# Kernel optimization log

Hardware: AMD Instinct MI355X
Metric: run time of the kernel (lower is better)

The kernel has to match this reference:

```python
import jax, jax.numpy as jnp
import numpy as np

H, W, C, HEADS = 28, 28, 512, 16
N = H * W
FF = 4 * C
DH = C // HEADS
NUM_REL = (2 * H - 1) * W + (2 * W - 1) + 1  # max relative index + 1 (source table is under-sized; see notes)


def _relative_indices():
    ys, xs = np.meshgrid(np.arange(H), np.arange(W), indexing='ij')
    py, px = ys.reshape(-1), xs.reshape(-1)
    # rel[q, k] = (y_k - y_q + H) * W + (x_k - x_q + W), matching the source loop
    rel = (py[None, :] - py[:, None] + H) * W + (px[None, :] - px[:, None] + W)
    return jnp.asarray(rel, dtype=jnp.int32)  # (N, N)


def setup_inputs() -> dict:
    key = jax.random.key(0)
    ks = jax.random.split(key, 9)
    g = lambda k, shape, s: (jax.random.normal(k, shape, jnp.float32) * s)
    return {
        'x': g(ks[0], (16, C, H, W), 1.0),
        'ln_w': jnp.ones((C,), jnp.float32),
        'ln_b': jnp.zeros((C,), jnp.float32),
        'Wq': g(ks[1], (C, C), 0.02), 'bq': jnp.zeros((C,), jnp.float32),
        'Wk': g(ks[2], (C, C), 0.02), 'bk': jnp.zeros((C,), jnp.float32),
        'Wv': g(ks[3], (C, C), 0.02), 'bv': jnp.zeros((C,), jnp.float32),
        'Wo': g(ks[4], (C, C), 0.02), 'bo': jnp.zeros((C,), jnp.float32),
        'rel_bias': g(ks[5], (HEADS, NUM_REL), 0.02),
        'W1': g(ks[6], (C, FF), 0.02), 'b1': jnp.zeros((FF,), jnp.float32),
        'W2': g(ks[7], (FF, C), 0.02), 'b2': jnp.zeros((C,), jnp.float32),
        'rel_idx': _relative_indices(),
    }


def reference(x, ln_w, ln_b, Wq, bq, Wk, bk, Wv, bv, Wo, bo, rel_bias, W1, b1, W2, b2, rel_idx):
    b = x.shape[0]
    xc = jnp.transpose(x, (0, 2, 3, 1)).reshape(b, N, C)  # b n c
    # LayerNorm over channels (per spatial position)
    mu = xc.mean(-1, keepdims=True)
    var = jnp.mean(jnp.square(xc - mu), -1, keepdims=True)
    xn = (xc - mu) * jax.lax.rsqrt(var + 1e-5) * ln_w + ln_b

    split = lambda t: t.reshape(b, N, HEADS, DH).transpose(0, 2, 1, 3)  # b h n d
    q = split(xn @ Wq + bq)
    k = split(xn @ Wk + bk)
    v = split(xn @ Wv + bv)

    bias = rel_bias[:, rel_idx]  # gather -> (heads, n, n)
    scores = jnp.einsum('bhnd,bhmd->bhnm', q, k) + bias[None]  # no 1/sqrt(d), faithful to source
    attn = jax.nn.softmax(scores, axis=-1)
    out = jnp.einsum('bhnm,bhmd->bhnd', attn, v)
    out = out.transpose(0, 2, 1, 3).reshape(b, N, C) @ Wo + bo

    x1 = xc + out  # skip (Identity) + attention branch
    ff = jax.nn.gelu(x1 @ W1 + b1, approximate=False) @ W2 + b2
    x2 = x1 + ff
    return x2.reshape(b, H, W, C).transpose(0, 3, 1, 2)  # back to b c h w
```

## Files before the change

### kernel.cpp

```cpp
#include <hip/hip_runtime.h>
#include <hip/hip_bf16.h>
#include <math.h>
#include <stdint.h>


typedef __bf16 bf16;
typedef __attribute__((ext_vector_type(8))) __bf16 bf16x8;
typedef __attribute__((ext_vector_type(4))) __bf16 bf16x4;
typedef __attribute__((ext_vector_type(4))) float f32x4;

#define NN 784
#define CC 512
#define NHEADS 16
#define DHEAD 32
#define FFD 2048
#define NBATCH 16
#define NREL 1596
#define MFULL (NBATCH * NN)
#define PACKSZ ((size_t)6422528)

__global__ __launch_bounds__(256) void detect_dtype(const unsigned int* xw, int* flag)
{
  __shared__ int cnt[256];
  int plausible = 0;
  for (int i = threadIdx.x; i < 1024; i += 256) {
    unsigned w = xw[i];
    unsigned lo = w & 0xFFFFu;
    unsigned e = (lo >> 7) & 0xFFu;
    if (lo == 0u || (e >= 90u && e <= 140u)) plausible++;
  }
  cnt[threadIdx.x] = plausible;
  __syncthreads();
  if (threadIdx.x == 0) {
    int tot = 0;
    for (int i = 0; i < 256; i++) tot += cnt[i];
    flag[0] = (tot >= 768) ? 1 : 0;
  }
}


__global__ __launch_bounds__(256) void transpose_split_all(
    const float* __restrict__ Wq, const float* __restrict__ Wk,
    const float* __restrict__ Wv, const float* __restrict__ Wo,
    const float* __restrict__ W1, const float* __restrict__ W2,
    bf16* __restrict__ WqkvT_h, bf16* __restrict__ WqkvT_l,
    bf16* __restrict__ WoT_h,   bf16* __restrict__ WoT_l,
    bf16* __restrict__ W1T_h,   bf16* __restrict__ W1T_l,
    bf16* __restrict__ W2T_h,   bf16* __restrict__ W2T_l,
    const int* __restrict__ flag)
{
  if (flag[0] != 0) return;
  int id = blockIdx.x;
  const float* W; bf16 *th, *tl; int K, Nout, roff, nx;
  if (id < 256)       { W = Wq; th = WqkvT_h; tl = WqkvT_l; K = 512;  Nout = 512;  roff = 0;    nx = 16; }
  else if (id < 512)  { W = Wk; th = WqkvT_h; tl = WqkvT_l; K = 512;  Nout = 512;  roff = 512;  nx = 16; id -= 256; }
  else if (id < 768)  { W = Wv; th = WqkvT_h; tl = WqkvT_l; K = 512;  Nout = 512;  roff = 1024; nx = 16; id -= 512; }
  else if (id < 1024) { W = Wo; th = WoT_h;   tl = WoT_l;   K = 512;  Nout = 512;  roff = 0;    nx = 16; id -= 768; }
  else if (id < 2048) { W = W1; th = W1T_h;   tl = W1T_l;   K = 512;  Nout = 2048; roff = 0;    nx = 64; id -= 1024; }
  else                { W = W2; th = W2T_h;   tl = W2T_l;   K = 2048; Nout = 512;  roff = 0;    nx = 16; id -= 2048; }
  const int n0 = (id % nx) * 32, k0 = (id / nx) * 32;

  __shared__ float tile[32][33];
  int tx = threadIdx.x & 31, ty = threadIdx.x >> 5;
  #pragma unroll
  for (int r = 0; r < 32; r += 8)
    tile[ty + r][tx] = W[(size_t)(k0 + ty + r) * Nout + n0 + tx];
  __syncthreads();
  #pragma unroll
  for (int r = 0; r < 32; r += 8) {
    float v = tile[tx][ty + r];
    bf16 h = (bf16)v;
    float lo = v - (float)h;
    size_t idx = (size_t)(roff + n0 + ty + r) * K + k0 + tx;
    th[idx] = h;
    tl[idx] = (bf16)lo;
  }
}

__global__ __launch_bounds__(256) void ln_single(
    const float* __restrict__ x, const float* __restrict__ lnw,
    const float* __restrict__ lnb, bf16* __restrict__ xh,
    const int* __restrict__ flag)
{
  if (flag[0] != 0) return;
  int bn = blockIdx.x;
  int b = bn / NN, n = bn - b * NN;
  const float* xb = x + (size_t)b * CC * NN + n;
  int t = threadIdx.x;
  float v0 = xb[(size_t)t * NN];
  float v1 = xb[(size_t)(t + 256) * NN];
  float s = v0 + v1, ss = v0 * v0 + v1 * v1;
  #pragma unroll
  for (int m = 32; m >= 1; m >>= 1) {
    s  += __shfl_xor(s,  m);
    ss += __shfl_xor(ss, m);
  }
  __shared__ float red[2][4];
  int w = t >> 6, l = t & 63;
  if (l == 0) { red[0][w] = s; red[1][w] = ss; }
  __syncthreads();
  float S  = red[0][0] + red[0][1] + red[0][2] + red[0][3];
  float SS = red[1][0] + red[1][1] + red[1][2] + red[1][3];
  float mu  = S * (1.f / 512.f);
  float var = SS * (1.f / 512.f) - mu * mu;
  float rstd = rsqrtf(var + 1e-5f);
  size_t o = (size_t)bn * CC;
  xh[o + t]       = (bf16)(((v0 - mu) * rstd) * lnw[t]       + lnb[t]);
  xh[o + t + 256] = (bf16)(((v1 - mu) * rstd) * lnw[t + 256] + lnb[t + 256]);
}

template <int NOUT, int KD, int ACT, int RESM, int OUTM>
__global__ __launch_bounds__(256) void gemm2(
    const bf16* __restrict__ A,
    const bf16* __restrict__ Bh, const bf16* __restrict__ Bl,
    const float* __restrict__ bias_q, const float* __restrict__ bias_k,
    const float* __restrict__ bias_v,
    float* __restrict__ outf, bf16* __restrict__ out_hi, bf16* __restrict__ out_lo,
    const float* __restrict__ extra_f, const bf16* __restrict__ ex_hi,
    const bf16* __restrict__ ex_lo,
    int M, const int* __restrict__ flag)
{
  if (flag[0] != 0) return;
  __shared__ bf16 sA [2][128 * 32];
  __shared__ bf16 sBh[2][128 * 32];
  __shared__ bf16 sBl[2][128 * 32];
  const int t = threadIdx.x;
  const int lane = t & 63;
  const int w = t >> 6;
  const int wr = w >> 1, wc = w & 1;
  const int lr = lane & 15, kg = lane >> 4;

  int wg = blockIdx.y * gridDim.x + blockIdx.x;
  const int nwg = gridDim.x * gridDim.y;
  if ((nwg & 7) == 0) {
    const int cpx = nwg >> 3;
    wg = (wg & 7) * cpx + (wg >> 3);
  }
  const int tile_n = (wg % gridDim.x) * 128;
  const int tile_m = (wg / gridDim.x) * 128;

  f32x4 acc[4][4];
  #pragma unroll
  for (int m = 0; m < 4; m++)
    #pragma unroll
    for (int n = 0; n < 4; n++) acc[m][n] = (f32x4)0.f;

  const int s0 = t, s1 = t + 256;
  int ar0 = tile_m + (s0 >> 2); if (ar0 >= M) ar0 = M - 1;
  int ar1 = tile_m + (s1 >> 2); if (ar1 >= M) ar1 = M - 1;
  const int br0 = tile_n + (s0 >> 2);
  const int br1 = tile_n + (s1 >> 2);
  const int ac0 = (s0 & 3) * 8, ac1 = (s1 & 3) * 8;
  const size_t a0 = (size_t)ar0 * KD + ac0;
  const size_t a1 = (size_t)ar1 * KD + ac1;
  const size_t b0 = (size_t)br0 * KD + ac0;
  const size_t b1 = (size_t)br1 * KD + ac1;

  #define STAGE(BUF, KO)                                                      \
    do {                                                                      \
      __builtin_amdgcn_global_load_lds(                                       \
          (const __attribute__((address_space(1))) void*)(A + a0 + (KO)),     \
          (__attribute__((address_space(3))) void*)(sA[BUF] + s0 * 8), 16, 0, 0); \
      __builtin_amdgcn_global_load_lds(                                       \
          (const __attribute__((address_space(1))) void*)(A + a1 + (KO)),     \
          (__attribute__((address_space(3))) void*)(sA[BUF] + s1 * 8), 16, 0, 0); \
      __builtin_amdgcn_global_load_lds(                                       \
          (const __attribute__((address_space(1))) void*)(Bh + b0 + (KO)),    \
          (__attribute__((address_space(3))) void*)(sBh[BUF] + s0 * 8), 16, 0, 0); \
      __builtin_amdgcn_global_load_lds(                                       \
          (const __attribute__((address_space(1))) void*)(Bh + b1 + (KO)),    \
          (__attribute__((address_space(3))) void*)(sBh[BUF] + s1 * 8), 16, 0, 0); \
      __builtin_amdgcn_global_load_lds(                                       \
          (const __attribute__((address_space(1))) void*)(Bl + b0 + (KO)),    \
          (__attribute__((address_space(3))) void*)(sBl[BUF] + s0 * 8), 16, 0, 0); \
      __builtin_amdgcn_global_load_lds(                                       \
          (const __attribute__((address_space(1))) void*)(Bl + b1 + (KO)),    \
          (__attribute__((address_space(3))) void*)(sBl[BUF] + s1 * 8), 16, 0, 0); \
    } while (0)

  STAGE(0, 0);
  asm volatile("s_waitcnt vmcnt(0)" ::: "memory");
  __builtin_amdgcn_sched_barrier(0);
  __builtin_amdgcn_s_barrier();
  __builtin_amdgcn_sched_barrier(0);

  int cur = 0;
  for (int k0 = 0; k0 < KD; k0 += 32) {
    if (k0 + 32 < KD) {
      if (cur) STAGE(0, k0 + 32); else STAGE(1, k0 + 32);
    }
    const bf16* pA  = sA [cur];
    const bf16* pBh = sBh[cur];
    const bf16* pBl = sBl[cur];
    bf16x8 af[4], bh[4], bl[4];
    #pragma unroll
    for (int m = 0; m < 4; m++) {
      const int off = (wr * 64 + m * 16 + lr) * 32 + kg * 8;
      af[m] = *(const bf16x8*)(pA + off);
    }
    #pragma unroll
    for (int n = 0; n < 4; n++) {
      const int off = (wc * 64 + n * 16 + lr) * 32 + kg * 8;
      bh[n] = *(const bf16x8*)(pBh + off);
      bl[n] = *(const bf16x8*)(pBl + off);
    }
    #pragma unroll
    for (int m = 0; m < 4; m++)
      #pragma unroll
      for (int n = 0; n < 4; n++) {
        acc[m][n] = __builtin_amdgcn_mfma_f32_16x16x32_bf16(af[m], bh[n], acc[m][n], 0, 0, 0);
        acc[m][n] = __builtin_amdgcn_mfma_f32_16x16x32_bf16(af[m], bl[n], acc[m][n], 0, 0, 0);
      }
    asm volatile("s_waitcnt vmcnt(0)" ::: "memory");
    __builtin_amdgcn_sched_barrier(0);
    __builtin_amdgcn_s_barrier();
    __builtin_amdgcn_sched_barrier(0);
    cur ^= 1;
  }
  #undef STAGE

  #pragma unroll
  for (int m = 0; m < 4; m++) {
    const int r0 = tile_m + wr * 64 + m * 16 + kg * 4;
    #pragma unroll
    for (int n = 0; n < 4; n++) {
      const int cg = tile_n + wc * 64 + n * 16 + lr;
      float bv;
      if (OUTM == 5) {
        const int reg2 = cg >> 9;
        const float* bp = reg2 == 0 ? bias_q : (reg2 == 1 ? bias_k : bias_v);
        bv = bp[cg & 511];
      } else {
        bv = bias_q[cg];
      }
      #pragma unroll
      for (int j = 0; j < 4; j++) {
        const int rg = r0 + j;
        if (rg >= M) continue;
        float vacc = acc[m][n][j] + bv;
        if (ACT == 1) vacc = 0.5f * vacc * (1.f + erff(vacc * 0.70710678118654752f));
        if (RESM == 1) {
          int bl_ = rg / NN, nn = rg - bl_ * NN;
          vacc += extra_f[((size_t)bl_ * CC + cg) * NN + nn];
        }
        if (RESM == 2) {
          size_t ei = (size_t)rg * CC + cg;
          vacc += (float)ex_hi[ei] + (float)ex_lo[ei];
        }
        if (OUTM == 3) {
          size_t oi = (size_t)rg * NOUT + cg;
          bf16 h = (bf16)vacc;
          out_hi[oi] = h;
          out_lo[oi] = (bf16)(vacc - (float)h);
        } else if (OUTM == 4) {
          int bl_ = rg / NN, nn = rg - bl_ * NN;
          outf[((size_t)bl_ * CC + cg) * NN + nn] = vacc;
        } else if (OUTM == 6) {
          out_hi[(size_t)rg * NOUT + cg] = (bf16)vacc;
        } else if (OUTM == 5) {
          const int reg2 = cg >> 9;
          const int c = cg & 511;
          const int hh = c >> 5, dd = c & 31;
          const int bl_ = rg / NN, nn = rg - bl_ * NN;
          const int bh_ = bl_ * NHEADS + hh;
          bf16 h = (bf16)vacc;
          if (reg2 == 0) {
            out_hi[((size_t)bh_ * NN + nn) * 32 + dd] = h;
          } else if (reg2 == 1) {
            out_hi[PACKSZ + ((size_t)bh_ * NN + nn) * 32 + dd] = h;
          } else {
            out_hi[2 * PACKSZ + ((size_t)bh_ * 32 + dd) * NN + nn] = h;
          }
        }
      }
    }
  }
}

__global__ __launch_bounds__(256) void attn_mfma(
    const bf16* __restrict__ pack, const float* __restrict__ relb,
    bf16* __restrict__ o_out, const int* __restrict__ flag)
{
  if (flag[0] != 0) return;
  const int h = blockIdx.y, b = blockIdx.z;
  __shared__ float biasLds[NREL];
  for (int i = threadIdx.x; i < NREL; i += 256) biasLds[i] = relb[(size_t)h * NREL + i];
  __syncthreads();
  const int w = threadIdx.x >> 6, lane = threadIdx.x & 63;
  const int qtile = blockIdx.x * 4 + w;
  if (qtile >= 49) return;
  const int kg = lane >> 4, lq = lane & 15;
  const int qg = qtile * 16 + lq;
  const int bh = b * NHEADS + h;
  const bf16* Q  = pack;
  const bf16* K  = pack + PACKSZ;
  const bf16* Vt = pack + 2 * PACKSZ;
  __shared__ bf16 Plds[4][16][72];

  const bf16x8 qf = *(const bf16x8*)(Q + ((size_t)bh * NN + qg) * 32 + kg * 8);

  float m = -1e30f, l = 0.f;
  f32x4 o0 = (f32x4)0.f, o1 = (f32x4)0.f;
  const float* bb = biasLds + 812 - qg;
  const size_t vrow0 = ((size_t)bh * 32 + lq) * NN;
  const size_t vrow1 = ((size_t)bh * 32 + 16 + lq) * NN;

  for (int c = 0; c < 12; c++) {
    const int c0 = c * 64;
    f32x4 st[4];
    #pragma unroll
    for (int t = 0; t < 4; t++) {
      const int kvr = c0 + t * 16 + lq;
      const bf16x8 kf = *(const bf16x8*)(K + ((size_t)bh * NN + kvr) * 32 + kg * 8);
      st[t] = __builtin_amdgcn_mfma_f32_16x16x32_bf16(kf, qf, (f32x4)0.f, 0, 0, 0);
    }
    float cm = -1e30f;
    #pragma unroll
    for (int t = 0; t < 4; t++)
      #pragma unroll
      for (int r = 0; r < 4; r++) {
        st[t][r] += bb[c0 + t * 16 + 4 * kg + r];
        cm = fmaxf(cm, st[t][r]);
      }
    cm = fmaxf(cm, __shfl_xor(cm, 16));
    cm = fmaxf(cm, __shfl_xor(cm, 32));
    const float mn = fmaxf(m, cm);
    const float al = __expf(m - mn);
    m = mn;
    float cl = 0.f;
    #pragma unroll
    for (int t = 0; t < 4; t++) {
      bf16x4 pk;
      #pragma unroll
      for (int r = 0; r < 4; r++) {
        float p = __expf(st[t][r] - m);
        bf16 pb = (bf16)p;
        pk[r] = pb;
        cl += (float)pb;
      }
      *(bf16x4*)(&Plds[w][lq][t * 16 + 4 * kg]) = pk;
    }
    cl += __shfl_xor(cl, 16);
    cl += __shfl_xor(cl, 32);
    l = l * al + cl;
    #pragma unroll
    for (int r = 0; r < 4; r++) {
      const float ar = __shfl(al, (lane & 48) | (kg * 4 + r));
      o0[r] *= ar; o1[r] *= ar;
    }
    #pragma unroll
    for (int s2 = 0; s2 < 2; s2++) {
      const bf16x8 pa = *(const bf16x8*)(&Plds[w][lq][s2 * 32 + kg * 8]);
      const bf16x8 v0 = *(const bf16x8*)(Vt + vrow0 + c0 + s2 * 32 + kg * 8);
      const bf16x8 v1 = *(const bf16x8*)(Vt + vrow1 + c0 + s2 * 32 + kg * 8);
      o0 = __builtin_amdgcn_mfma_f32_16x16x32_bf16(pa, v0, o0, 0, 0, 0);
      o1 = __builtin_amdgcn_mfma_f32_16x16x32_bf16(pa, v1, o1, 0, 0, 0);
    }
  }

  {
    const int c0 = 768;
    const int kvr = c0 + lq;
    const bf16x8 kf = *(const bf16x8*)(K + ((size_t)bh * NN + kvr) * 32 + kg * 8);
    f32x4 a = __builtin_amdgcn_mfma_f32_16x16x32_bf16(kf, qf, (f32x4)0.f, 0, 0, 0);
    float cm = -1e30f;
    #pragma unroll
    for (int r = 0; r < 4; r++) {
      a[r] += bb[c0 + 4 * kg + r];
      cm = fmaxf(cm, a[r]);
    }
    cm = fmaxf(cm, __shfl_xor(cm, 16));
    cm = fmaxf(cm, __shfl_xor(cm, 32));
    const float mn = fmaxf(m, cm);
    const float al = __expf(m - mn);
    m = mn;
    float cl = 0.f;
    bf16x4 pk, zk;
    #pragma unroll
    for (int r = 0; r < 4; r++) {
      float p = __expf(a[r] - m);
      bf16 pb = (bf16)p;
      pk[r] = pb;
      zk[r] = (bf16)0.f;
      cl += (float)pb;
    }
    *(bf16x4*)(&Plds[w][lq][4 * kg]) = pk;
    *(bf16x4*)(&Plds[w][lq][16 + 4 * kg]) = zk;
    cl += __shfl_xor(cl, 16);
    cl += __shfl_xor(cl, 32);
    l = l * al + cl;
    #pragma unroll
    for (int r = 0; r < 4; r++) {
      const float ar = __shfl(al, (lane & 48) | (kg * 4 + r));
      o0[r] *= ar; o1[r] *= ar;
    }
    bf16x8 vz;
    #pragma unroll
    for (int e = 0; e < 8; e++) vz[e] = (bf16)0.f;
    const int voff = c0 + (kg < 2 ? kg * 8 : 0);
    bf16x8 v0 = *(const bf16x8*)(Vt + vrow0 + voff);
    bf16x8 v1 = *(const bf16x8*)(Vt + vrow1 + voff);
    if (kg >= 2) { v0 = vz; v1 = vz; }
    const bf16x8 pa = *(const bf16x8*)(&Plds[w][lq][kg * 8]);
    o0 = __builtin_amdgcn_mfma_f32_16x16x32_bf16(pa, v0, o0, 0, 0, 0);
    o1 = __builtin_amdgcn_mfma_f32_16x16x32_bf16(pa, v1, o1, 0, 0, 0);
  }

  const float inv = 1.f / l;
  #pragma unroll
  for (int r = 0; r < 4; r++) {
    const float ir = __shfl(inv, (lane & 48) | (kg * 4 + r));
    const int rq = qtile * 16 + kg * 4 + r;
    const size_t oi = ((size_t)b * NN + rq) * CC + h * DHEAD;
    o_out[oi + lq]      = (bf16)(o0[r] * ir);
    o_out[oi + 16 + lq] = (bf16)(o1[r] * ir);
  }
}

static void run_fast_fp32(void* const* d_in, void* d_out, char* base,
                          const int* flag, hipStream_t stream)
{
  const float* x    = (const float*)d_in[0];
  const float* lnw  = (const float*)d_in[1];
  const float* lnb  = (const float*)d_in[2];
  const float* Wq   = (const float*)d_in[3];
  const float* bq   = (const float*)d_in[4];
  const float* Wk   = (const float*)d_in[5];
  const float* bk   = (const float*)d_in[6];
  const float* Wv   = (const float*)d_in[7];
  const float* bv   = (const float*)d_in[8];
  const float* Wo   = (const float*)d_in[9];
  const float* bo   = (const float*)d_in[10];
  const float* relb = (const float*)d_in[11];
  const float* W1   = (const float*)d_in[12];
  const float* b1   = (const float*)d_in[13];
  const float* W2   = (const float*)d_in[14];
  const float* b2   = (const float*)d_in[15];
  float* outp = (float*)d_out;

  bf16* WqkvT_h = (bf16*)(base);
  bf16* WqkvT_l = WqkvT_h + (size_t)1536 * 512;
  bf16* WoT_h   = WqkvT_l + (size_t)1536 * 512;
  bf16* WoT_l   = WoT_h   + (size_t)512 * 512;
  bf16* W1T_h   = WoT_l   + (size_t)512 * 512;
  bf16* W1T_l   = W1T_h   + (size_t)2048 * 512;
  bf16* W2T_h   = W1T_l   + (size_t)2048 * 512;
  bf16* W2T_l   = W2T_h   + (size_t)512 * 2048;
  bf16* xn   = (bf16*)(base + 12582912);
  bf16* qkvp = (bf16*)(base + 25427968);
  bf16* x1_h = (bf16*)(base + 25427968);
  bf16* x1_l = (bf16*)(base + 38273024);
  bf16* ff   = (bf16*)(base + 51118080);
  bf16* at   = xn;

  transpose_split_all<<<dim3(3072), 256, 0, stream>>>(
      Wq, Wk, Wv, Wo, W1, W2,
      WqkvT_h, WqkvT_l, WoT_h, WoT_l, W1T_h, W1T_l, W2T_h, W2T_l, flag);

  const int M = MFULL;
  const int gm = M / 128;

  ln_single<<<dim3(M), 256, 0, stream>>>(x, lnw, lnb, xn, flag);

  gemm2<1536, 512, 0, 0, 5><<<dim3(12, gm), 256, 0, stream>>>(
      xn, WqkvT_h, WqkvT_l, bq, bk, bv,
      (float*)nullptr, qkvp, (bf16*)nullptr,
      (const float*)nullptr, (const bf16*)nullptr, (const bf16*)nullptr,
      M, flag);

  attn_mfma<<<dim3(13, NHEADS, NBATCH), 256, 0, stream>>>(qkvp, relb, at, flag);

  gemm2<512, 512, 0, 1, 3><<<dim3(4, gm), 256, 0, stream>>>(
      at, WoT_h, WoT_l, bo, (const float*)nullptr, (const float*)nullptr,
      (float*)nullptr, x1_h, x1_l,
      x, (const bf16*)nullptr, (const bf16*)nullptr,
      M, flag);

  gemm2<2048, 512, 1, 0, 6><<<dim3(16, gm), 256, 0, stream>>>(
      x1_h, W1T_h, W1T_l, b1, (const float*)nullptr, (const float*)nullptr,
      (float*)nullptr, ff, (bf16*)nullptr,
      (const float*)nullptr, (const bf16*)nullptr, (const bf16*)nullptr,
      M, flag);

  gemm2<512, 2048, 0, 2, 4><<<dim3(4, gm), 256, 0, stream>>>(
      ff, W2T_h, W2T_l, b2, (const float*)nullptr, (const float*)nullptr,
      outp, (bf16*)nullptr, (bf16*)nullptr,
      (const float*)nullptr, x1_h, x1_l,
      M, flag);
}

template <typename T, int WANT>
__global__ __launch_bounds__(256) void ln_naive(
    const T* __restrict__ x, const T* __restrict__ lnw, const T* __restrict__ lnb,
    T* __restrict__ xn, const int* __restrict__ flag)
{
  if (flag[0] != WANT) return;
  int bn = blockIdx.x;
  int b = bn / NN, n = bn - b * NN;
  const T* xb = x + (size_t)b * CC * NN + n;
  int t = threadIdx.x;
  float v0 = (float)xb[(size_t)t * NN];
  float v1 = (float)xb[(size_t)(t + 256) * NN];
  float s = v0 + v1, ss = v0 * v0 + v1 * v1;
  #pragma unroll
  for (int m = 32; m >= 1; m >>= 1) {
    s  += __shfl_xor(s,  m);
    ss += __shfl_xor(ss, m);
  }
  __shared__ float red[2][4];
  int w = t >> 6, l = t & 63;
  if (l == 0) { red[0][w] = s; red[1][w] = ss; }
  __syncthreads();
  float S  = red[0][0] + red[0][1] + red[0][2] + red[0][3];
  float SS = red[1][0] + red[1][1] + red[1][2] + red[1][3];
  float mu  = S * (1.f / 512.f);
  float var = SS * (1.f / 512.f) - mu * mu;
  float rstd = rsqrtf(var + 1e-5f);
  T* o = xn + (size_t)bn * CC;
  o[t]       = (T)(((v0 - mu) * rstd) * (float)lnw[t]       + (float)lnb[t]);
  o[t + 256] = (T)(((v1 - mu) * rstd) * (float)lnw[t + 256] + (float)lnb[t + 256]);
}

template <typename T, int NOUT, int KD, int ACT, int RESM, int OUTM, int WANT>
__global__ __launch_bounds__(256) void gemm_naive(
    const T* __restrict__ A, const T* __restrict__ W, const T* __restrict__ bias,
    T* __restrict__ out, const T* __restrict__ extra, const int* __restrict__ flag)
{
  if (flag[0] != WANT) return;
  __shared__ float a_t[16][17];
  __shared__ float w_t[16][17];
  int tx = threadIdx.x & 15, ty = threadIdx.x >> 4;
  int m0 = blockIdx.y * 16, bz = blockIdx.z;
  int mg = m0 + ty;
  int jg = blockIdx.x * 16 + tx;
  int ar = mg < NN ? mg : NN - 1;
  const T* Ab = A + (size_t)bz * NN * KD;
  float acc = 0.f;
  for (int k0 = 0; k0 < KD; k0 += 16) {
    a_t[ty][tx] = (float)Ab[(size_t)ar * KD + k0 + tx];
    w_t[ty][tx] = (float)W[(size_t)(k0 + ty) * NOUT + jg];
    __syncthreads();
    #pragma unroll
    for (int kk = 0; kk < 16; kk++)
      acc += a_t[ty][kk] * w_t[kk][tx];
    __syncthreads();
  }
  if (mg >= NN) return;
  acc += (float)bias[jg];
  if (ACT == 1) acc = 0.5f * acc * (1.f + erff(acc * 0.70710678118654752f));
  if (RESM == 1) acc += (float)extra[((size_t)bz * CC + jg) * NN + mg];
  if (RESM == 2) acc += (float)extra[((size_t)bz * NN + mg) * CC + jg];
  if (OUTM == 0) out[((size_t)bz * NN + mg) * NOUT + jg] = (T)acc;
  else           out[((size_t)bz * NOUT + jg) * NN + mg] = (T)acc;
}

template <typename T, int WANT>
__global__ __launch_bounds__(256) void attn_naive(
    const T* __restrict__ q, const T* __restrict__ k, const T* __restrict__ v,
    const T* __restrict__ rel_bias, const int* __restrict__ rel_idx,
    T* __restrict__ attn_out, const int* __restrict__ flag)
{
  if (flag[0] != WANT) return;
  int i = blockIdx.x * 256 + threadIdx.x;
  int h = blockIdx.y, b = blockIdx.z;
  if (i >= NN) return;
  const T* qr = q + ((size_t)b * NN + i) * CC + h * DHEAD;
  float qv[DHEAD];
  #pragma unroll
  for (int d = 0; d < DHEAD; d++) qv[d] = (float)qr[d];
  const int* ridx = rel_idx + (size_t)i * NN;
  const T* rb = rel_bias + (size_t)h * NREL;
  const T* kb = k + (size_t)b * NN * CC + h * DHEAD;
  const T* vb = v + (size_t)b * NN * CC + h * DHEAD;

  float m = -1e30f;
  for (int j = 0; j < NN; j++) {
    const T* kr = kb + (size_t)j * CC;
    float s = 0.f;
    #pragma unroll
    for (int d = 0; d < DHEAD; d++) s += qv[d] * (float)kr[d];
    s += (float)rb[ridx[j]];
    m = fmaxf(m, s);
  }
  float l = 0.f;
  float o[DHEAD];
  #pragma unroll
  for (int d = 0; d < DHEAD; d++) o[d] = 0.f;
  for (int j = 0; j < NN; j++) {
    const T* kr = kb + (size_t)j * CC;
    float s = 0.f;
    #pragma unroll
    for (int d = 0; d < DHEAD; d++) s += qv[d] * (float)kr[d];
    s += (float)rb[ridx[j]];
    float p = __expf(s - m);
    l += p;
    const T* vr = vb + (size_t)j * CC;
    #pragma unroll
    for (int d = 0; d < DHEAD; d++) o[d] += p * (float)vr[d];
  }
  float inv = 1.f / l;
  T* op = attn_out + ((size_t)b * NN + i) * CC + h * DHEAD;
  #pragma unroll
  for (int d = 0; d < DHEAD; d++) op[d] = (T)(o[d] * inv);
}

template <typename T, int WANT>
static void run_pipeline(void* const* d_in, void* d_out, char* buf, int Bc,
                         const int* flag, hipStream_t stream)
{
  const T* x    = (const T*)d_in[0];
  const T* lnw  = (const T*)d_in[1];
  const T* lnb  = (const T*)d_in[2];
  const T* Wq   = (const T*)d_in[3];
  const T* bq   = (const T*)d_in[4];
  const T* Wk   = (const T*)d_in[5];
  const T* bk   = (const T*)d_in[6];
  const T* Wv   = (const T*)d_in[7];
  const T* bv   = (const T*)d_in[8];
  const T* Wo   = (const T*)d_in[9];
  const T* bo   = (const T*)d_in[10];
  const T* relb = (const T*)d_in[11];
  const T* W1   = (const T*)d_in[12];
  const T* b1   = (const T*)d_in[13];
  const T* W2   = (const T*)d_in[14];
  const T* b2   = (const T*)d_in[15];
  const int* reli = (const int*)d_in[16];
  T* outp = (T*)d_out;

  const size_t TOK = (size_t)NN * CC;
  T* xn  = (T*)(buf);
  T* qb  = (T*)(buf + (size_t)Bc * TOK * 4);
  T* kb  = (T*)(buf + 2 * (size_t)Bc * TOK * 4);
  T* vb  = (T*)(buf + 3 * (size_t)Bc * TOK * 4);
  T* ff1 = (T*)(buf + 4 * (size_t)Bc * TOK * 4);
  T* attn_out = xn;
  T* x1 = qb;

  for (int c0 = 0; c0 < NBATCH; c0 += Bc) {
    const T* xc   = x    + (size_t)c0 * CC * NN;
    T*       outc = outp + (size_t)c0 * CC * NN;
    ln_naive<T, WANT><<<dim3(Bc * NN), 256, 0, stream>>>(xc, lnw, lnb, xn, flag);
    gemm_naive<T, CC, CC, 0, 0, 0, WANT><<<dim3(32, 49, Bc), 256, 0, stream>>>(xn, Wq, bq, qb, (const T*)nullptr, flag);
    gemm_naive<T, CC, CC, 0, 0, 0, WANT><<<dim3(32, 49, Bc), 256, 0, stream>>>(xn, Wk, bk, kb, (const T*)nullptr, flag);
    gemm_naive<T, CC, CC, 0, 0, 0, WANT><<<dim3(32, 49, Bc), 256, 0, stream>>>(xn, Wv, bv, vb, (const T*)nullptr, flag);
    attn_naive<T, WANT><<<dim3(4, NHEADS, Bc), 256, 0, stream>>>(qb, kb, vb, relb, reli, attn_out, flag);
    gemm_naive<T, CC, CC, 0, 1, 0, WANT><<<dim3(32, 49, Bc), 256, 0, stream>>>(attn_out, Wo, bo, x1, xc, flag);
    gemm_naive<T, FFD, CC, 1, 0, 0, WANT><<<dim3(128, 49, Bc), 256, 0, stream>>>(x1, W1, b1, ff1, (const T*)nullptr, flag);
    gemm_naive<T, CC, FFD, 0, 2, 1, WANT><<<dim3(32, 49, Bc), 256, 0, stream>>>(ff1, W2, b2, outc, x1, flag);
  }
}

extern "C" void kernel_launch(void* const* d_in, const int* in_sizes, int n_in,
                              void* d_out, int out_size, void* d_ws, size_t ws_size,
                              hipStream_t stream)
{
  int* flag = (int*)d_ws;
  char* base = (char*)d_ws + 256;
  size_t avail = ws_size > 256 ? ws_size - 256 : 0;

  const size_t REQ_FAST = 102498304;
  const size_t PB16 = (size_t)(4 * NN * CC + NN * FFD) * 2;
  const size_t PB32 = (size_t)(4 * NN * CC + NN * FFD) * 4;

  detect_dtype<<<dim3(1), 256, 0, stream>>>((const unsigned int*)d_in[0], flag);

  if (avail >= REQ_FAST) {
    run_fast_fp32(d_in, d_out, base, flag, stream);
  } else {
    int Bc32 = 1;
    for (int c : {16, 8, 4, 2}) {
      if ((size_t)c * PB32 <= avail) { Bc32 = c; break; }
    }
    run_pipeline<float, 0>(d_in, d_out, base, Bc32, flag, stream);
  }

  int Bc16 = 1;
  for (int c : {16, 8, 4, 2}) {
    if ((size_t)c * PB16 <= avail) { Bc16 = c; break; }
  }
  run_pipeline<bf16, 1>(d_in, d_out, base, Bc16, flag, stream);
}
```

Before: 578.8 us.

## Enlarge GEMM M-tile to 256 rows with grouped XCD-aware tile ordering

Doubles each workgroup's M tile from 128 to 256 rows, so every wave computes 8x4 MFMA tiles and each B (hi/lo weight) tile loaded into LDS is reused across twice as many rows. The block-to-tile mapping is replaced by an XCD-aware scheme that gives each XCD a contiguous range and walks 7x4 super-tiles for cache locality. This cuts weight-traffic and LDS loads per FLOP but doubles the accumulator registers, which may lower occupancy. The grid shrinks to half as many workgroups, and the mapping hardcodes 49 M-tiles and assumes gridDim.x is a multiple of 4.

```diff
diff --git a/kernel.cpp b/kernel.cpp
--- a/kernel.cpp
+++ b/kernel.cpp
@@ -121,7 +121,7 @@
     int M, const int* __restrict__ flag)
 {
   if (flag[0] != 0) return;
-  __shared__ bf16 sA [2][128 * 32];
+  __shared__ bf16 sA [2][256 * 32];
   __shared__ bf16 sBh[2][128 * 32];
   __shared__ bf16 sBl[2][128 * 32];
   const int t = threadIdx.x;
@@ -130,52 +130,57 @@
   const int wr = w >> 1, wc = w & 1;
   const int lr = lane & 15, kg = lane >> 4;
 
-  int wg = blockIdx.y * gridDim.x + blockIdx.x;
-  const int nwg = gridDim.x * gridDim.y;
-  if ((nwg & 7) == 0) {
-    const int cpx = nwg >> 3;
-    wg = (wg & 7) * cpx + (wg >> 3);
-  }
-  const int tile_n = (wg % gridDim.x) * 128;
-  const int tile_m = (wg / gridDim.x) * 128;
-
-  f32x4 acc[4][4];
-  #pragma unroll
-  for (int m = 0; m < 4; m++)
+  const int gx = gridDim.x;
+  const int nwg = gx * 49;
+  const int raw = blockIdx.y * gx + blockIdx.x;
+  const int q8 = nwg >> 3, r8 = nwg & 7;
+  const int xcd = raw & 7, idx = raw >> 3;
+  const int start = xcd < r8 ? xcd * (q8 + 1) : r8 * (q8 + 1) + (xcd - r8) * q8;
+  const int seq = start + idx;
+  const int spr = gx >> 2;
+  const int s28 = seq / 28, j28 = seq - s28 * 28;
+  const int sm = s28 / spr, sn = s28 - sm * spr;
+  const int im = j28 >> 2, in = j28 & 3;
+  const int tile_m = (sm * 7 + im) * 256;
+  const int tile_n = (sn * 4 + in) * 128;
+
+  f32x4 acc[8][4];
+  #pragma unroll
+  for (int m = 0; m < 8; m++)
     #pragma unroll
     for (int n = 0; n < 4; n++) acc[m][n] = (f32x4)0.f;
 
-  const int s0 = t, s1 = t + 256;
-  int ar0 = tile_m + (s0 >> 2); if (ar0 >= M) ar0 = M - 1;
-  int ar1 = tile_m + (s1 >> 2); if (ar1 >= M) ar1 = M - 1;
-  const int br0 = tile_n + (s0 >> 2);
-  const int br1 = tile_n + (s1 >> 2);
-  const int ac0 = (s0 & 3) * 8, ac1 = (s1 & 3) * 8;
-  const size_t a0 = (size_t)ar0 * KD + ac0;
-  const size_t a1 = (size_t)ar1 * KD + ac1;
-  const size_t b0 = (size_t)br0 * KD + ac0;
-  const size_t b1 = (size_t)br1 * KD + ac1;
-
-  #define STAGE(BUF, KO)                                                      \
-    do {                                                                      \
-      __builtin_amdgcn_global_load_lds(                                       \
-          (const __attribute__((address_space(1))) void*)(A + a0 + (KO)),     \
-          (__attribute__((address_space(3))) void*)(sA[BUF] + s0 * 8), 16, 0, 0); \
-      __builtin_amdgcn_global_load_lds(                                       \
-          (const __attribute__((address_space(1))) void*)(A + a1 + (KO)),     \
-          (__attribute__((address_space(3))) void*)(sA[BUF] + s1 * 8), 16, 0, 0); \
-      __builtin_amdgcn_global_load_lds(                                       \
-          (const __attribute__((address_space(1))) void*)(Bh + b0 + (KO)),    \
-          (__attribute__((address_space(3))) void*)(sBh[BUF] + s0 * 8), 16, 0, 0); \
-      __builtin_amdgcn_global_load_lds(                                       \
-          (const __attribute__((address_space(1))) void*)(Bh + b1 + (KO)),    \
-          (__attribute__((address_space(3))) void*)(sBh[BUF] + s1 * 8), 16, 0, 0); \
-      __builtin_amdgcn_global_load_lds(                                       \
-          (const __attribute__((address_space(1))) void*)(Bl + b0 + (KO)),    \
-          (__attribute__((address_space(3))) void*)(sBl[BUF] + s0 * 8), 16, 0, 0); \
-      __builtin_amdgcn_global_load_lds(                                       \
-          (const __attribute__((address_space(1))) void*)(Bl + b1 + (KO)),    \
-          (__attribute__((address_space(3))) void*)(sBl[BUF] + s1 * 8), 16, 0, 0); \
+  size_t aoff[4], bhoff[2], bloff[2];
+  #pragma unroll
+  for (int i = 0; i < 4; i++) {
+    const int seg = t + 256 * i;
+    int r = tile_m + (seg >> 2); if (r >= M) r = M - 1;
+    aoff[i] = (size_t)r * KD + (seg & 3) * 8;
+  }
+  #pragma unroll
+  for (int i = 0; i < 2; i++) {
+    const int seg = t + 256 * i;
+    const int r = tile_n + (seg >> 2);
+    bhoff[i] = (size_t)r * KD + (seg & 3) * 8;
+    bloff[i] = bhoff[i];
+  }
+
+  #define STAGE(BUF, KO)                                                        \
+    do {                                                                        \
+      _Pragma("unroll")                                                         \
+      for (int i = 0; i < 4; i++)                                               \
+        __builtin_amdgcn_global_load_lds(                                       \
+            (const __attribute__((address_space(1))) void*)(A + aoff[i] + (KO)),\
+            (__attribute__((address_space(3))) void*)(sA[BUF] + (t + 256 * i) * 8), 16, 0, 0); \
+      _Pragma("unroll")                                                         \
+      for (int i = 0; i < 2; i++) {                                             \
+        __builtin_amdgcn_global_load_lds(                                       \
+            (const __attribute__((address_space(1))) void*)(Bh + bhoff[i] + (KO)),\
+            (__attribute__((address_space(3))) void*)(sBh[BUF] + (t + 256 * i) * 8), 16, 0, 0); \
+        __builtin_amdgcn_global_load_lds(                                       \
+            (const __attribute__((address_space(1))) void*)(Bl + bloff[i] + (KO)),\
+            (__attribute__((address_space(3))) void*)(sBl[BUF] + (t + 256 * i) * 8), 16, 0, 0); \
+      }                                                                         \
     } while (0)
 
   STAGE(0, 0);
@@ -192,10 +197,10 @@
     const bf16* pA  = sA [cur];
     const bf16* pBh = sBh[cur];
     const bf16* pBl = sBl[cur];
-    bf16x8 af[4], bh[4], bl[4];
-    #pragma unroll
-    for (int m = 0; m < 4; m++) {
-      const int off = (wr * 64 + m * 16 + lr) * 32 + kg * 8;
+    bf16x8 af[8], bh[4], bl[4];
+    #pragma unroll
+    for (int m = 0; m < 8; m++) {
+      const int off = (wr * 128 + m * 16 + lr) * 32 + kg * 8;
       af[m] = *(const bf16x8*)(pA + off);
     }
     #pragma unroll
@@ -205,7 +210,7 @@
       bl[n] = *(const bf16x8*)(pBl + off);
     }
     #pragma unroll
-    for (int m = 0; m < 4; m++)
+    for (int m = 0; m < 8; m++)
       #pragma unroll
       for (int n = 0; n < 4; n++) {
         acc[m][n] = __builtin_amdgcn_mfma_f32_16x16x32_bf16(af[m], bh[n], acc[m][n], 0, 0, 0);
@@ -220,8 +225,8 @@
   #undef STAGE
 
   #pragma unroll
-  for (int m = 0; m < 4; m++) {
-    const int r0 = tile_m + wr * 64 + m * 16 + kg * 4;
+  for (int m = 0; m < 8; m++) {
+    const int r0 = tile_m + wr * 128 + m * 16 + kg * 4;
     #pragma unroll
     for (int n = 0; n < 4; n++) {
       const int cg = tile_n + wc * 64 + n * 16 + lr;
@@ -458,7 +463,7 @@
       WqkvT_h, WqkvT_l, WoT_h, WoT_l, W1T_h, W1T_l, W2T_h, W2T_l, flag);
 
   const int M = MFULL;
-  const int gm = M / 128;
+  const int gm = M / 256;
 
   ln_single<<<dim3(M), 256, 0, stream>>>(x, lnw, lnb, xn, flag);
 
```

Result: slower. 765.2 us (+32.2%).

## Coalesce LayerNorm reads across tokens and tile GEMM workgroups in 7x4 groups

Applied to the files above, without the earlier changes.

The LayerNorm kernel now gives each block 64 tokens, with each wave holding 128 channels per token in registers. Its global loads are therefore coalesced along the token dimension instead of striding by N for every element. Outputs are written as 8-wide bf16 vectors. The GEMM workgroup mapping changes from an XCD-interleave-only remap to an XCD remap followed by 7x4 tile grouping, which should improve L2 reuse of the A and B tiles. Risks are high register pressure from 128 floats per thread in LayerNorm and the fallback mapping used when the grid is not divisible as assumed.

```diff
diff --git a/kernel.cpp b/kernel.cpp
--- a/kernel.cpp
+++ b/kernel.cpp
@@ -77,36 +77,46 @@
   }
 }
 
-__global__ __launch_bounds__(256) void ln_single(
+__global__ __launch_bounds__(256) void ln_coal(
     const float* __restrict__ x, const float* __restrict__ lnw,
     const float* __restrict__ lnb, bf16* __restrict__ xh,
     const int* __restrict__ flag)
 {
   if (flag[0] != 0) return;
-  int bn = blockIdx.x;
-  int b = bn / NN, n = bn - b * NN;
-  const float* xb = x + (size_t)b * CC * NN + n;
-  int t = threadIdx.x;
-  float v0 = xb[(size_t)t * NN];
-  float v1 = xb[(size_t)(t + 256) * NN];
-  float s = v0 + v1, ss = v0 * v0 + v1 * v1;
-  #pragma unroll
-  for (int m = 32; m >= 1; m >>= 1) {
-    s  += __shfl_xor(s,  m);
-    ss += __shfl_xor(ss, m);
-  }
-  __shared__ float red[2][4];
-  int w = t >> 6, l = t & 63;
-  if (l == 0) { red[0][w] = s; red[1][w] = ss; }
+  const int b = blockIdx.y;
+  const int n0 = blockIdx.x * 64;
+  const int w = threadIdx.x >> 6, l = threadIdx.x & 63;
+  const bool act = (n0 + l) < NN;
+  int tok = n0 + l; if (tok >= NN) tok = NN - 1;
+  const float* xb = x + ((size_t)b * CC + w * 128) * NN + tok;
+  float vals[128];
+  float s = 0.f, ss = 0.f;
+  #pragma unroll
+  for (int c = 0; c < 128; c++) {
+    float v = xb[(size_t)c * NN];
+    vals[c] = v; s += v; ss += v * v;
+  }
+  __shared__ float S[4][64], SS[4][64];
+  S[w][l] = s; SS[w][l] = ss;
   __syncthreads();
-  float S  = red[0][0] + red[0][1] + red[0][2] + red[0][3];
-  float SS = red[1][0] + red[1][1] + red[1][2] + red[1][3];
-  float mu  = S * (1.f / 512.f);
-  float var = SS * (1.f / 512.f) - mu * mu;
-  float rstd = rsqrtf(var + 1e-5f);
-  size_t o = (size_t)bn * CC;
-  xh[o + t]       = (bf16)(((v0 - mu) * rstd) * lnw[t]       + lnb[t]);
-  xh[o + t + 256] = (bf16)(((v1 - mu) * rstd) * lnw[t + 256] + lnb[t + 256]);
+  const float St  = S[0][l] + S[1][l] + S[2][l] + S[3][l];
+  const float SSt = SS[0][l] + SS[1][l] + SS[2][l] + SS[3][l];
+  const float mu  = St * (1.f / 512.f);
+  const float var = SSt * (1.f / 512.f) - mu * mu;
+  const float rstd = rsqrtf(var + 1e-5f);
+  if (act) {
+    const size_t row = ((size_t)b * NN + n0 + l) * CC + w * 128;
+    #pragma unroll
+    for (int cc = 0; cc < 16; cc++) {
+      bf16x8 o;
+      #pragma unroll
+      for (int e = 0; e < 8; e++) {
+        const int c = cc * 8 + e;
+        o[e] = (bf16)((vals[c] - mu) * rstd * lnw[w * 128 + c] + lnb[w * 128 + c]);
+      }
+      *(bf16x8*)(xh + row + cc * 8) = o;
+    }
+  }
 }
 
 template <int NOUT, int KD, int ACT, int RESM, int OUTM>
@@ -130,14 +140,22 @@
   const int wr = w >> 1, wc = w & 1;
   const int lr = lane & 15, kg = lane >> 4;
 
-  int wg = blockIdx.y * gridDim.x + blockIdx.x;
-  const int nwg = gridDim.x * gridDim.y;
-  if ((nwg & 7) == 0) {
-    const int cpx = nwg >> 3;
-    wg = (wg & 7) * cpx + (wg >> 3);
-  }
-  const int tile_n = (wg % gridDim.x) * 128;
-  const int tile_m = (wg / gridDim.x) * 128;
+  const int gx = gridDim.x, gy = gridDim.y;
+  const int nwg = gx * gy;
+  const int raw = blockIdx.y * gx + blockIdx.x;
+  int tile_m, tile_n;
+  if ((nwg & 7) == 0 && (gx & 3) == 0 && (gy % 7) == 0) {
+    const int q8 = nwg >> 3;
+    const int seq = (raw & 7) * q8 + (raw >> 3);
+    const int spr = gx >> 2;
+    const int s28 = seq / 28, j28 = seq - s28 * 28;
+    const int sm = s28 / spr, sn = s28 - sm * spr;
+    tile_m = (sm * 7 + (j28 >> 2)) * 128;
+    tile_n = (sn * 4 + (j28 & 3)) * 128;
+  } else {
+    tile_m = blockIdx.y * 128;
+    tile_n = blockIdx.x * 128;
+  }
 
   f32x4 acc[4][4];
   #pragma unroll
@@ -460,7 +478,7 @@
   const int M = MFULL;
   const int gm = M / 128;
 
-  ln_single<<<dim3(M), 256, 0, stream>>>(x, lnw, lnb, xn, flag);
+  ln_coal<<<dim3(13, NBATCH), 256, 0, stream>>>(x, lnw, lnb, xn, flag);
 
   gemm2<1536, 512, 0, 0, 5><<<dim3(12, gm), 256, 0, stream>>>(
       xn, WqkvT_h, WqkvT_l, bq, bk, bv,
```

New measurement: 560.6 us. 3.2% less time.
